# Optimization experiments

Measured on AMD Instinct MI355X. Metric: run time of the kernel, lower is better.

The kernel has to match this reference:

```python
import jax, jax.numpy as jnp
import numpy as np

T = 2048            # flattened tokens (vLLM style)
D = 4096            # hidden_size
NSSM = 128          # ssm_state_size
K = 4               # conv kernel size
G = 8               # n_groups
H = 128             # mamba_num_heads
P = 64              # mamba_head_dim
INTER = H * P       # 8192 = expand * hidden_size
CONV_DIM = INTER + 2 * G * NSSM   # 10240 (x, B, C share the conv)
PROJ = INTER + CONV_DIM + H       # 18560 (z, xBC, dt)
Q = 128             # SSD chunk size
EPS = 1e-5


def setup_inputs() -> dict:
    key = jax.random.key(0)
    ks = jax.random.split(key, 9)
    s = 0.02
    return {
        "hidden_states": jax.random.normal(ks[0], (T, D), jnp.float32),
        "residual": jax.random.normal(ks[1], (T, D), jnp.float32),
        "norm_w": jnp.ones((D,), jnp.float32),
        "in_proj_w": jax.random.normal(ks[2], (PROJ, D), jnp.float32) * s,
        "conv_w": jax.random.normal(ks[3], (CONV_DIM, K), jnp.float32) * 0.2,
        "conv_b": jax.random.normal(ks[4], (CONV_DIM,), jnp.float32) * 0.1,
        "A_log": jnp.log(jax.random.uniform(ks[5], (H,), jnp.float32, 1.0, 16.0)),
        "D_res": jax.random.normal(ks[6], (H,), jnp.float32) * 0.5 + 1.0,
        "dt_bias": jax.random.normal(ks[7], (H,), jnp.float32) * 0.5,
        "gn_w": jnp.ones((INTER,), jnp.float32),
        "out_proj_w": jax.random.normal(ks[8], (D, INTER), jnp.float32) * s,
    }


def _forward(hidden_states, residual, norm_w, in_proj_w, conv_w, conv_b,
             A_log, D_res, dt_bias, gn_w, out_proj_w):
    # ---- fused add + RMSNorm (vLLM RMSNorm(hidden, residual)) ----
    resid = hidden_states + residual
    hs = resid * jax.lax.rsqrt(jnp.mean(resid * resid, -1, keepdims=True) + EPS) * norm_w

    # ---- MambaMixer2 ----
    proj = hs @ in_proj_w.T                              # [T, PROJ]
    z, xBC, dt = jnp.split(proj, [INTER, INTER + CONV_DIM], axis=-1)

    # causal depthwise conv1d over time + SiLU
    xp = jnp.pad(xBC, ((K - 1, 0), (0, 0)))
    conv = conv_b + sum(conv_w[:, k] * xp[k:k + T] for k in range(K))
    xBC = jax.nn.silu(conv)

    x, B, C = jnp.split(xBC, [INTER, INTER + G * NSSM], axis=-1)
    x = x.reshape(T, H, P)
    Bh = jnp.repeat(B.reshape(T, G, NSSM), H // G, axis=1)   # [T,H,N]
    Ch = jnp.repeat(C.reshape(T, G, NSSM), H // G, axis=1)   # [T,H,N]

    dt = jax.nn.softplus(dt + dt_bias)                   # [T,H]
    A = -jnp.exp(A_log)                                  # [H] (negative)

    # ---- SSD chunked selective scan ----
    NC = T // Q
    a = (dt * A).reshape(NC, Q, H)                       # per-step log decay (<=0)
    cum = jnp.cumsum(a, axis=1)                          # inclusive cumsum, [NC,Q,H]
    Xd = (dt[:, :, None] * x).reshape(NC, Q, H, P)
    Bc = Bh.reshape(NC, Q, H, NSSM)
    Cc = Ch.reshape(NC, Q, H, NSSM)

    # intra-chunk: Y[i] = sum_{j<=i} (C_i.B_j) exp(cum_i-cum_j) Xd_j
    CB = jnp.einsum('cqhn,ckhn->chqk', Cc, Bc)
    cumT = cum.transpose(0, 2, 1)                        # [NC,H,Q]
    mask = jnp.tril(jnp.ones((Q, Q), bool))
    Lm = jnp.where(mask, jnp.exp(cumT[:, :, :, None] - cumT[:, :, None, :]), 0.0)
    Y = jnp.einsum('chqk,ckhp->cqhp', CB * Lm, Xd)

    # chunk-local end states, then scan states across chunks
    cum_end = cum[:, -1]                                 # [NC,H]
    decay_out = jnp.exp(cum_end[:, None] - cum)          # [NC,Q,H]
    S_loc = jnp.einsum('cqhn,cqh,cqhp->chnp', Bc, decay_out, Xd)
    chunk_decay = jnp.exp(cum_end)                       # [NC,H]

    def step(s, inp):
        dec, sl = inp
        return dec[:, None, None] * s + sl, s            # emit state BEFORE chunk

    _, S_prev = jax.lax.scan(step, jnp.zeros((H, NSSM, P), x.dtype),
                             (chunk_decay, S_loc))       # [NC,H,N,P]

    # inter-chunk contribution + skip connection D*x
    Y = Y + jnp.einsum('cqhn,cqh,chnp->cqhp', Cc, jnp.exp(cum), S_prev)
    y = Y.reshape(T, H, P) + D_res[None, :, None] * x

    # gated RMSNorm then out projection
    y = y.reshape(T, INTER) * jax.nn.silu(z)
    y = y * jax.lax.rsqrt(jnp.mean(y * y, -1, keepdims=True) + EPS) * gn_w
    return y @ out_proj_w.T, resid


def reference(hidden_states, residual, norm_w, in_proj_w, conv_w, conv_b,
              A_log, D_res, dt_bias, gn_w, out_proj_w):
    return _forward(hidden_states, residual, norm_w, in_proj_w, conv_w, conv_b,
                    A_log, D_res, dt_bias, gn_w, out_proj_w)
```

## Files before the change

kernel.cpp:

```cpp
#include <hip/hip_runtime.h>
#include <stdint.h>

typedef unsigned short u16;
typedef unsigned int   u32;
typedef float  f32x4  __attribute__((ext_vector_type(4)));
typedef __bf16 bf16x8 __attribute__((ext_vector_type(8)));
typedef u16    u16x4  __attribute__((ext_vector_type(4)));
typedef u16    u16x8  __attribute__((ext_vector_type(8)));

#define T_N     2048
#define D_N     4096
#define H_N     128
#define P_N     64
#define G_N     8
#define NS_N    128
#define INTER_N 8192
#define CONVD_N 10240
#define PROJ_N  18560
#define NGEMM_N 18432
#define NC_N    16

__device__ __forceinline__ float bf2f(u16 u){ u32 x = ((u32)u) << 16; return __builtin_bit_cast(float, x); }
__device__ __forceinline__ u16 f2bf(float f){
  u32 u = __builtin_bit_cast(u32, f);
  u += 0x7FFFu + ((u >> 16) & 1u);
  return (u16)(u >> 16);
}

__device__ __forceinline__ void gld_lds16(const void* g, void* lds){
  __builtin_amdgcn_global_load_lds(
      (const __attribute__((address_space(1))) void*)(uintptr_t)g,
      (__attribute__((address_space(3))) void*)(u32)(uintptr_t)lds,
      16, 0, 0);
}

__global__ __launch_bounds__(256)
void k_addnorm(const float* __restrict__ hin, const float* __restrict__ rin,
               const float* __restrict__ nw, float* __restrict__ resid,
               u16* __restrict__ hs16, float* __restrict__ rstd){
  __shared__ float red[4];
  const int row = blockIdx.x, tid = threadIdx.x;
  const size_t rb = (size_t)row * D_N;
  f32x4 s[4];
  float ss = 0.f;
  #pragma unroll
  for (int i = 0; i < 4; ++i){
    int c4 = tid + i*256;
    f32x4 a = *(const f32x4*)&hin[rb + (size_t)c4*4];
    f32x4 b = *(const f32x4*)&rin[rb + (size_t)c4*4];
    s[i] = a + b;
    *(f32x4*)&resid[rb + (size_t)c4*4] = s[i];
    ss += s[i][0]*s[i][0] + s[i][1]*s[i][1] + s[i][2]*s[i][2] + s[i][3]*s[i][3];
  }
  #pragma unroll
  for (int o = 32; o > 0; o >>= 1) ss += __shfl_down(ss, o, 64);
  if ((tid & 63) == 0) red[tid >> 6] = ss;
  __syncthreads();
  float tot = (red[0] + red[1]) + (red[2] + red[3]);
  float rs = rsqrtf(tot / (float)D_N + 1e-5f);
  if (tid == 0) rstd[row] = rs;
  #pragma unroll
  for (int i = 0; i < 4; ++i){
    int c4 = tid + i*256;
    f32x4 w = *(const f32x4*)&nw[(size_t)c4*4];
    u16x4 o = { f2bf(s[i][0]*rs*w[0]), f2bf(s[i][1]*rs*w[1]),
                f2bf(s[i][2]*rs*w[2]), f2bf(s[i][3]*rs*w[3]) };
    *(u16x4*)&hs16[rb + (size_t)c4*4] = o;
  }
}

__global__ void k_cvt(const float* __restrict__ in, u16* __restrict__ out, size_t n4){
  size_t i = (size_t)blockIdx.x * blockDim.x + threadIdx.x;
  size_t stride = (size_t)gridDim.x * blockDim.x;
  for (; i < n4; i += stride){
    f32x4 v = *(const f32x4*)&in[i*4];
    u16x4 o = { f2bf(v[0]), f2bf(v[1]), f2bf(v[2]), f2bf(v[3]) };
    *(u16x4*)&out[i*4] = o;
  }
}

__global__ void k_wdt(const float* __restrict__ W, const float* __restrict__ nw,
                      float* __restrict__ Wn){
  int idx = blockIdx.x*256 + threadIdx.x;
  int d = idx >> 7, h = idx & 127;
  Wn[(size_t)d*128 + h] = W[(size_t)(INTER_N + CONVD_N + h)*D_N + d] * nw[d];
}

__global__ __launch_bounds__(256)
void k_dtgemm(const float* __restrict__ resid, const float* __restrict__ Wn,
              float* __restrict__ dtpart){
  __shared__ float lhs[16*128];
  const int tid = threadIdx.x;
  const int tb = blockIdx.x >> 3, ks = blockIdx.x & 7;
  const int t0 = tb * 16;
  const int k0 = ks * (D_N / 8);
  const int hcol = tid & 127, rh = tid >> 7;
  float acc[8] = {0,0,0,0,0,0,0,0};
  for (int kt = k0; kt < k0 + D_N/8; kt += 128){
    __syncthreads();
    #pragma unroll
    for (int it = 0; it < 2; ++it){
      int idx = it*256 + tid;
      int rr = idx >> 5, c4 = idx & 31;
      *(f32x4*)&lhs[rr*128 + c4*4] = *(const f32x4*)&resid[(size_t)(t0+rr)*D_N + kt + c4*4];
    }
    __syncthreads();
    #pragma unroll 4
    for (int kk4 = 0; kk4 < 32; ++kk4){
      f32x4 w4;
      #pragma unroll
      for (int j = 0; j < 4; ++j) w4[j] = Wn[(size_t)(kt + kk4*4 + j)*128 + hcol];
      #pragma unroll
      for (int j = 0; j < 8; ++j){
        f32x4 lv = *(const f32x4*)&lhs[(rh*8 + j)*128 + kk4*4];
        acc[j] += lv[0]*w4[0] + lv[1]*w4[1] + lv[2]*w4[2] + lv[3]*w4[3];
      }
    }
  }
  #pragma unroll
  for (int j = 0; j < 8; ++j){
    int t = t0 + rh*8 + j;
    dtpart[((size_t)ks*T_N + t)*128 + hcol] = acc[j];
  }
}

__global__ void k_dtprep(const float* __restrict__ dtpart, const float* __restrict__ rstd,
                         const float* __restrict__ dt_bias, const float* __restrict__ A_log,
                         float* __restrict__ dtv, float* __restrict__ cum,
                         float* __restrict__ cumend, float* __restrict__ dec){
  int c = blockIdx.x, h = threadIdx.x;
  float A = -expf(A_log[h]);
  float bias = dt_bias[h];
  float cm = 0.f;
  for (int q = 0; q < 128; ++q){
    int t = c*128 + q;
    float s = 0.f;
    #pragma unroll
    for (int kspl = 0; kspl < 8; ++kspl)
      s += dtpart[((size_t)kspl*T_N + t)*128 + h];
    float x = s * rstd[t] + bias;
    float dv = (x > 20.f) ? x : log1pf(expf(x));
    dtv[(size_t)t*128 + h] = dv;
    cm += dv * A;
    cum[(size_t)t*128 + h] = cm;
  }
  cumend[c*128 + h] = cm;
  dec[c*128 + h] = expf(cm);
}

#define STA(BUF,HH,KT) gld_lds16(pA + (size_t)((HH)*32)*K + (size_t)(KT)*64, shb + (BUF)*BSZ + (HH)*4096 + tid*16)
#define STB(BUF,HH,KT) gld_lds16(pB + (size_t)((HH)*32)*K + (size_t)(KT)*64, shb + (BUF)*BSZ + 16384 + (HH)*4096 + tid*16)
#define VMWN do { asm volatile("s_waitcnt vmcnt(%0)" :: "n"(NF) : "memory"); __builtin_amdgcn_sched_barrier(0); } while(0)
#define RDA4(BUF, MOFF)                                                                 \
    bf16x8 a0 = *(const bf16x8*)(shb + (BUF)*BSZ + rdA + (MOFF)*2048 + sA0);            \
    bf16x8 a1 = *(const bf16x8*)(shb + (BUF)*BSZ + rdA + (MOFF)*2048 + sA1);            \
    bf16x8 a2 = *(const bf16x8*)(shb + (BUF)*BSZ + rdA + ((MOFF)+1)*2048 + sA0);        \
    bf16x8 a3 = *(const bf16x8*)(shb + (BUF)*BSZ + rdA + ((MOFF)+1)*2048 + sA1);
#define RDBALL(BUF, BB)                                                                 \
    _Pragma("unroll") for (int nn = 0; nn < NF; ++nn){                                  \
      BB[nn][0] = *(const bf16x8*)(shb + (BUF)*BSZ + rdB + nn*2048 + sA0);              \
      BB[nn][1] = *(const bf16x8*)(shb + (BUF)*BSZ + rdB + nn*2048 + sA1);              \
    }
#define MM24(MOFF, BB)                                                                  \
    _Pragma("unroll") for (int nn = 0; nn < NF; ++nn)                                   \
      acc[(MOFF)+0][nn] = __builtin_amdgcn_mfma_f32_16x16x32_bf16(a0, BB[nn][0], acc[(MOFF)+0][nn],0,0,0); \
    _Pragma("unroll") for (int nn = 0; nn < NF; ++nn)                                   \
      acc[(MOFF)+1][nn] = __builtin_amdgcn_mfma_f32_16x16x32_bf16(a2, BB[nn][0], acc[(MOFF)+1][nn],0,0,0); \
    _Pragma("unroll") for (int nn = 0; nn < NF; ++nn)                                   \
      acc[(MOFF)+0][nn] = __builtin_amdgcn_mfma_f32_16x16x32_bf16(a1, BB[nn][1], acc[(MOFF)+0][nn],0,0,0); \
    _Pragma("unroll") for (int nn = 0; nn < NF; ++nn)                                   \
      acc[(MOFF)+1][nn] = __builtin_amdgcn_mfma_f32_16x16x32_bf16(a3, BB[nn][1], acc[(MOFF)+1][nn],0,0,0);
#define ENDPH                                                                           \
    __builtin_amdgcn_s_setprio(0);                                                      \
    __builtin_amdgcn_s_barrier();                                                       \
    __builtin_amdgcn_sched_barrier(0);

template<int NF, typename OT>
__global__ __launch_bounds__(256, 2)
void k_gemmw(const u16* __restrict__ A, const u16* __restrict__ Bm,
             OT* __restrict__ C, int ldc, int K, int nkt){
  constexpr int BSZ = 16384 + NF*4096;
  __shared__ char shb[2*BSZ];
  const int tid = threadIdx.x, ln = tid & 63, wid = tid >> 6;
  const int wm = wid >> 1, wn = wid & 1;
  const int lr = ln & 15, lg = ln >> 4;

  const int gx = gridDim.x;
  const int mt = gridDim.y;
  const int lin = blockIdx.y * gx + blockIdx.x;
  const int xcd = lin & 7, sub = lin >> 3;
  const int ncx = gx >> 3;
  const int n_local = sub / mt;
  const int m_idx   = sub % mt;
  const int m0 = m_idx << 7;
  const int n0 = (xcd * ncx + n_local) * (NF*32);

  const int srow = tid >> 3;
  const int slog = ((tid & 7) ^ (srow & 7)) * 8;
  const u16* pA = A + (size_t)(m0 + srow)*K + slog;
  const u16* pB = Bm + (size_t)(n0 + srow)*K + slog;

  const int sA0 = (lg ^ (ln & 7)) << 4;
  const int sA1 = ((4 + lg) ^ (ln & 7)) << 4;
  const u32 rdA = wm*8192 + lr*128;
  const u32 rdB = 16384 + wn*(NF*2048) + lr*128;

  f32x4 acc[4][NF] = {};

  STA(0,0,0); STA(0,1,0); STA(0,2,0); STA(0,3,0);
  #pragma unroll
  for (int hh = 0; hh < NF; ++hh) STB(0, hh, 0);
  #pragma unroll
  for (int hh = 0; hh < NF; ++hh) STB(1, hh, 1);
  VMWN;
  __builtin_amdgcn_s_barrier();
  __builtin_amdgcn_sched_barrier(0);

  const int nit = nkt >> 1;
  #pragma unroll 1
  for (int it = 0; it < nit; ++it){
    const int t1 = 2*it + 1;
    int t2 = 2*it + 2; if (t2 >= nkt) t2 = 0;
    int t3 = 2*it + 3; if (t3 >= nkt) t3 = 1;
    bf16x8 bb0[NF][2], bb1[NF][2];
    {
      RDA4(0, 0) RDBALL(0, bb0)
      STA(1,0,t1); STA(1,1,t1); STA(1,2,t1); STA(1,3,t1);
      __builtin_amdgcn_s_setprio(1);
      MM24(0, bb0)
      ENDPH
    }
    {
      RDA4(0, 2)
      #pragma unroll
      for (int hh = 0; hh < NF; ++hh) STB(0, hh, t2);
      VMWN;
      __builtin_amdgcn_s_setprio(1);
      MM24(2, bb0)
      ENDPH
    }
    {
      RDA4(1, 0) RDBALL(1, bb1)
      STA(0,0,t2); STA(0,1,t2); STA(0,2,t2); STA(0,3,t2);
      __builtin_amdgcn_s_setprio(1);
      MM24(0, bb1)
      ENDPH
    }
    {
      RDA4(1, 2)
      #pragma unroll
      for (int hh = 0; hh < NF; ++hh) STB(1, hh, t3);
      VMWN;
      __builtin_amdgcn_s_setprio(1);
      MM24(2, bb1)
      ENDPH
    }
  }
  asm volatile("s_waitcnt vmcnt(0)" ::: "memory");

  const int crow = m0 + wm*64 + lg*4;
  const int ccol = n0 + wn*(NF*16) + lr;
  #pragma unroll
  for (int m = 0; m < 4; ++m)
    #pragma unroll
    for (int nn = 0; nn < NF; ++nn)
      #pragma unroll
      for (int r = 0; r < 4; ++r){
        float v = acc[m][nn][r];
        if constexpr (__is_same(OT, float))
          C[(size_t)(crow + m*16 + r)*ldc + ccol + nn*16] = v;
        else
          C[(size_t)(crow + m*16 + r)*ldc + ccol + nn*16] = f2bf(v);
      }
}

__global__ __launch_bounds__(256)
void k_conv(const u16* __restrict__ proj16, const float* __restrict__ cw,
            const float* __restrict__ cb, u16* __restrict__ x16,
            u16* __restrict__ B16, u16* __restrict__ C16){
  const int ch = blockIdx.x*256 + threadIdx.x;
  const int tbase = blockIdx.y*64;
  f32x4 w = *(const f32x4*)&cw[(size_t)ch*4];
  const float bias = cb[ch];
  const u16* pcol = proj16 + INTER_N + ch;
  float p0 = 0.f, p1 = 0.f, p2 = 0.f;
  if (tbase >= 3){
    p0 = bf2f(pcol[(size_t)(tbase-3)*PROJ_N]);
    p1 = bf2f(pcol[(size_t)(tbase-2)*PROJ_N]);
    p2 = bf2f(pcol[(size_t)(tbase-1)*PROJ_N]);
  }
  u16* xdst = (ch < INTER_N) ? x16 + ch
            : (ch < INTER_N + 1024) ? B16 + (ch - INTER_N)
            : C16 + (ch - INTER_N - 1024);
  const int dstride = (ch < INTER_N) ? INTER_N : 1024;
  #pragma unroll 4
  for (int i = 0; i < 64; ++i){
    int t = tbase + i;
    float cur = bf2f(pcol[(size_t)t*PROJ_N]);
    float acc = bias + w[0]*p0 + w[1]*p1 + w[2]*p2 + w[3]*cur;
    float v = acc / (1.f + __expf(-acc));
    xdst[(size_t)t*dstride] = f2bf(v);
    p0 = p1; p1 = p2; p2 = cur;
  }
}

__global__ __launch_bounds__(512)
void k_ssda(const u16* __restrict__ B16, const u16* __restrict__ x16,
            const float* __restrict__ dtv, const float* __restrict__ cum,
            const float* __restrict__ cumend, u16* __restrict__ SlocT){
  __shared__ u16 lBdT[128*136];
  __shared__ u16 lXdT[64*136];
  __shared__ float lDec[128], lDt[128];
  const int tid = threadIdx.x, wid = tid >> 6, ln = tid & 63;
  const int c = blockIdx.x >> 7, h = blockIdx.x & 127, g = h >> 4;
  if (tid < 128){
    int t = c*128 + tid;
    lDec[tid] = __expf(cumend[c*128 + h] - cum[(size_t)t*128 + h]);
    lDt[tid]  = dtv[(size_t)t*128 + h];
  }
  __syncthreads();
  for (int it = 0; it < 32; ++it){
    int idx = it*512 + tid;
    int q = idx >> 7, n = idx & 127;
    float bv = bf2f(B16[(size_t)(c*128 + q)*1024 + g*128 + n]) * lDec[q];
    lBdT[n*136 + q] = f2bf(bv);
  }
  for (int it = 0; it < 16; ++it){
    int idx = it*512 + tid;
    int q = idx >> 6, p = idx & 63;
    float xv = bf2f(x16[(size_t)(c*128 + q)*INTER_N + h*64 + p]) * lDt[q];
    lXdT[p*136 + q] = f2bf(xv);
  }
  __syncthreads();
  const int wr = wid >> 1, wc = wid & 1;
  const int kofs = (ln >> 4) << 3;
  f32x4 acc[2][2] = {};
  #pragma unroll
  for (int ks = 0; ks < 4; ++ks){
    bf16x8 a[2], b[2];
    #pragma unroll
    for (int m = 0; m < 2; ++m) a[m] = *(const bf16x8*)&lBdT[(wr*32 + m*16 + (ln & 15))*136 + ks*32 + kofs];
    #pragma unroll
    for (int n = 0; n < 2; ++n) b[n] = *(const bf16x8*)&lXdT[(wc*32 + n*16 + (ln & 15))*136 + ks*32 + kofs];
    #pragma unroll
    for (int m = 0; m < 2; ++m)
      #pragma unroll
      for (int n = 0; n < 2; ++n)
        acc[m][n] = __builtin_amdgcn_mfma_f32_16x16x32_bf16(a[m], b[n], acc[m][n], 0, 0, 0);
  }
  const size_t base = (size_t)(c*128 + h) * 8192;
  #pragma unroll
  for (int m = 0; m < 2; ++m)
    #pragma unroll
    for (int n = 0; n < 2; ++n){
      int p  = wc*32 + n*16 + (ln & 15);
      int nn = wr*32 + m*16 + ((ln >> 4) << 2);
      u16x4 o = { f2bf(acc[m][n][0]), f2bf(acc[m][n][1]), f2bf(acc[m][n][2]), f2bf(acc[m][n][3]) };
      *(u16x4*)&SlocT[base + (size_t)p*128 + nn] = o;
    }
}

__global__ __launch_bounds__(256)
void k_scan(const u16* __restrict__ SlocT, const float* __restrict__ dec,
            u16* __restrict__ SprevT){
  int idx = blockIdx.x*256 + threadIdx.x;
  int h = idx >> 10, p = (idx >> 4) & 63, n8 = (idx & 15)*8;
  float s[8] = {};
  for (int c = 0; c < NC_N; ++c){
    size_t off = (size_t)(c*128 + h)*8192 + (size_t)p*128 + n8;
    u16x8 o;
    #pragma unroll
    for (int j = 0; j < 8; ++j) o[j] = f2bf(s[j]);
    *(u16x8*)&SprevT[off] = o;
    u16x8 sl = *(const u16x8*)&SlocT[off];
    float d = dec[c*128 + h];
    #pragma unroll
    for (int j = 0; j < 8; ++j) s[j] = d*s[j] + bf2f(sl[j]);
  }
}

__global__ __launch_bounds__(512)
void k_ssdb(const u16* __restrict__ C16, const u16* __restrict__ B16g,
            const u16* __restrict__ x16, const float* __restrict__ dtv,
            const float* __restrict__ cum, const u16* __restrict__ SprevT,
            const u16* __restrict__ proj16, const float* __restrict__ Dres,
            u16* __restrict__ yg16){
  __shared__ u16 lC[128*136];
  __shared__ u16 lBP[128*136];
  __shared__ u16 lXdT[64*136];
  __shared__ float lCum[128], lDt[128];
  const int tid = threadIdx.x, wid = tid >> 6, ln = tid & 63;
  const int c = blockIdx.x >> 7, h = blockIdx.x & 127, g = h >> 4;
  if (tid < 128){
    int t = c*128 + tid;
    lCum[tid] = cum[(size_t)t*128 + h];
    lDt[tid]  = dtv[(size_t)t*128 + h];
  }
  __syncthreads();
  #pragma unroll
  for (int it = 0; it < 4; ++it){
    int idx = it*512 + tid;
    int q = idx >> 4, n8 = (idx & 15) << 3;
    size_t gi = (size_t)(c*128 + q)*1024 + g*128 + n8;
    *(u16x8*)&lC[q*136 + n8]  = *(const u16x8*)&C16[gi];
    *(u16x8*)&lBP[q*136 + n8] = *(const u16x8*)&B16g[gi];
  }
  for (int it = 0; it < 16; ++it){
    int idx = it*512 + tid;
    int q = idx >> 6, p = idx & 63;
    lXdT[p*136 + q] = f2bf(bf2f(x16[(size_t)(c*128 + q)*INTER_N + h*64 + p]) * lDt[q]);
  }
  __syncthreads();
  const int kofs = (ln >> 4) << 3;
  {
    const int wr = wid >> 2, wc = wid & 3;
    f32x4 cb[4][2] = {};
    #pragma unroll
    for (int ks = 0; ks < 4; ++ks){
      bf16x8 a[4], b[2];
      #pragma unroll
      for (int m = 0; m < 4; ++m) a[m] = *(const bf16x8*)&lC[(wr*64 + m*16 + (ln & 15))*136 + ks*32 + kofs];
      #pragma unroll
      for (int n = 0; n < 2; ++n) b[n] = *(const bf16x8*)&lBP[(wc*32 + n*16 + (ln & 15))*136 + ks*32 + kofs];
      #pragma unroll
      for (int m = 0; m < 4; ++m)
        #pragma unroll
        for (int n = 0; n < 2; ++n)
          cb[m][n] = __builtin_amdgcn_mfma_f32_16x16x32_bf16(a[m], b[n], cb[m][n], 0, 0, 0);
    }
    __syncthreads();
    #pragma unroll
    for (int m = 0; m < 4; ++m)
      #pragma unroll
      for (int n = 0; n < 2; ++n){
        int kcol = (wid & 3)*32 + n*16 + (ln & 15);
        float ck = lCum[kcol];
        #pragma unroll
        for (int r = 0; r < 4; ++r){
          int q = (wid >> 2)*64 + m*16 + ((ln >> 4) << 2) + r;
          float v = (kcol <= q) ? cb[m][n][r] * __expf(lCum[q] - ck) : 0.f;
          lBP[q*136 + kcol] = f2bf(v);
        }
      }
  }
  __syncthreads();
  const int yr = wid >> 1, yc = wid & 1;
  f32x4 y1[2][2] = {}, y2[2][2] = {};
  const size_t spbase = (size_t)(c*128 + h) * 8192;
  #pragma unroll
  for (int ks = 0; ks < 4; ++ks){
    bf16x8 ap[2], acf[2], bx[2], bs[2];
    #pragma unroll
    for (int m = 0; m < 2; ++m){
      int qr = yr*32 + m*16 + (ln & 15);
      ap[m]  = *(const bf16x8*)&lBP[qr*136 + ks*32 + kofs];
      acf[m] = *(const bf16x8*)&lC [qr*136 + ks*32 + kofs];
    }
    #pragma unroll
    for (int n = 0; n < 2; ++n){
      int p = yc*32 + n*16 + (ln & 15);
      bx[n] = *(const bf16x8*)&lXdT[p*136 + ks*32 + kofs];
      bs[n] = *(const bf16x8*)&SprevT[spbase + (size_t)p*128 + ks*32 + kofs];
    }
    #pragma unroll
    for (int m = 0; m < 2; ++m)
      #pragma unroll
      for (int n = 0; n < 2; ++n){
        y1[m][n] = __builtin_amdgcn_mfma_f32_16x16x32_bf16(ap[m],  bx[n], y1[m][n], 0, 0, 0);
        y2[m][n] = __builtin_amdgcn_mfma_f32_16x16x32_bf16(acf[m], bs[n], y2[m][n], 0, 0, 0);
      }
  }
  const float dh = Dres[h];
  #pragma unroll
  for (int m = 0; m < 2; ++m)
    #pragma unroll
    for (int r = 0; r < 4; ++r){
      int q = yr*32 + m*16 + ((ln >> 4) << 2) + r;
      float eq = __expf(lCum[q]);
      size_t t = (size_t)(c*128 + q);
      #pragma unroll
      for (int n = 0; n < 2; ++n){
        int p = yc*32 + n*16 + (ln & 15);
        int chn = h*64 + p;
        float xv = bf2f(x16[t*INTER_N + chn]);
        float zv = bf2f(proj16[t*PROJ_N + chn]);
        float yv = y1[m][n][r] + eq*y2[m][n][r] + dh*xv;
        float sg = zv / (1.f + __expf(-zv));
        yg16[t*INTER_N + chn] = f2bf(yv * sg);
      }
    }
}

__global__ __launch_bounds__(256)
void k_gnorm(const u16* __restrict__ yg, const float* __restrict__ gnw,
             u16* __restrict__ yn16){
  __shared__ float red[4];
  const int row = blockIdx.x, tid = threadIdx.x;
  const u16* rp = yg + (size_t)row * INTER_N;
  u16x8 v[4];
  float ss = 0.f;
  #pragma unroll
  for (int i = 0; i < 4; ++i){
    v[i] = *(const u16x8*)&rp[(size_t)(tid + i*256)*8];
    #pragma unroll
    for (int j = 0; j < 8; ++j){ float f = bf2f(v[i][j]); ss += f*f; }
  }
  #pragma unroll
  for (int o = 32; o > 0; o >>= 1) ss += __shfl_down(ss, o, 64);
  if ((tid & 63) == 0) red[tid >> 6] = ss;
  __syncthreads();
  float tot = (red[0] + red[1]) + (red[2] + red[3]);
  float sc = rsqrtf(tot / (float)INTER_N + 1e-5f);
  #pragma unroll
  for (int i = 0; i < 4; ++i){
    int c8 = (tid + i*256)*8;
    u16x8 o;
    #pragma unroll
    for (int j = 0; j < 8; ++j)
      o[j] = f2bf(bf2f(v[i][j]) * sc * gnw[c8 + j]);
    *(u16x8*)&yn16[(size_t)row*INTER_N + c8] = o;
  }
}

extern "C" void kernel_launch(void* const* d_in, const int* in_sizes, int n_in,
                              void* d_out, int out_size, void* d_ws, size_t ws_size,
                              hipStream_t stream){
  (void)in_sizes; (void)n_in; (void)out_size;
  const float* hs_in     = (const float*)d_in[0];
  const float* res_in    = (const float*)d_in[1];
  const float* norm_w    = (const float*)d_in[2];
  const float* in_proj_w = (const float*)d_in[3];
  const float* conv_w    = (const float*)d_in[4];
  const float* conv_b    = (const float*)d_in[5];
  const float* A_log     = (const float*)d_in[6];
  const float* D_res     = (const float*)d_in[7];
  const float* dt_bias   = (const float*)d_in[8];
  const float* gn_w      = (const float*)d_in[9];
  const float* out_proj_w= (const float*)d_in[10];

  float* out0      = (float*)d_out;
  float* resid_out = out0 + (size_t)T_N * D_N;

  char* ws = (char*)d_ws;
  const size_t o_hs16   = 0;
  const size_t o_Win16  = 16777216;
  const size_t o_Wout16 = 168820736;
  const size_t o_proj   = 235929600;
  const size_t o_Wn     = 387973120;
  const size_t o_dtv    = 391118848;
  const size_t o_cum    = 392167424;
  const size_t o_cumend = 393216000;
  const size_t o_dec    = 393224192;
  const size_t o_rstd   = 393232384;
  const size_t o_x16    = 393240576;
  const size_t o_B16    = 426795008;
  const size_t o_C16    = 430989312;
  const size_t o_SlocT  = 435183616;
  const size_t o_SprevT = 468738048;
  const size_t o_yn16   = 502292480;
  const size_t WS_NEED  = 535846912;
  if (ws_size < WS_NEED) return;

  u16*   hs16   = (u16*)  (ws + o_hs16);
  u16*   Win16  = (u16*)  (ws + o_Win16);
  u16*   Wout16 = (u16*)  (ws + o_Wout16);
  u16*   proj16 = (u16*)  (ws + o_proj);
  float* Wn     = (float*)(ws + o_Wn);
  float* dtpart = (float*)(ws + o_proj);
  float* dtv    = (float*)(ws + o_dtv);
  float* cum    = (float*)(ws + o_cum);
  float* cumend = (float*)(ws + o_cumend);
  float* dec    = (float*)(ws + o_dec);
  float* rstd   = (float*)(ws + o_rstd);
  u16*   x16    = (u16*)  (ws + o_x16);
  u16*   B16    = (u16*)  (ws + o_B16);
  u16*   C16    = (u16*)  (ws + o_C16);
  u16*   SlocT  = (u16*)  (ws + o_SlocT);
  u16*   SprevT = (u16*)  (ws + o_SprevT);
  u16*   yn16   = (u16*)  (ws + o_yn16);
  u16*   yg16   = (u16*)  (ws + o_Win16);

  k_addnorm<<<T_N, 256, 0, stream>>>(hs_in, res_in, norm_w, resid_out, hs16, rstd);
  k_cvt<<<4096, 256, 0, stream>>>(in_proj_w,  Win16,  (size_t)NGEMM_N * D_N / 4);
  k_cvt<<<2048, 256, 0, stream>>>(out_proj_w, Wout16, (size_t)D_N * INTER_N / 4);
  k_wdt<<<2048, 256, 0, stream>>>(in_proj_w, norm_w, Wn);
  k_dtgemm<<<1024, 256, 0, stream>>>(resid_out, Wn, dtpart);
  k_dtprep<<<NC_N, 128, 0, stream>>>(dtpart, rstd, dt_bias, A_log, dtv, cum, cumend, dec);
  k_gemmw<6, u16><<<dim3(NGEMM_N/192, T_N/128), 256, 0, stream>>>(hs16, Win16, proj16, PROJ_N, D_N, D_N/64);
  k_conv<<<dim3(CONVD_N/256, T_N/64), 256, 0, stream>>>(proj16, conv_w, conv_b, x16, B16, C16);
  k_ssda<<<NC_N * H_N, 512, 0, stream>>>(B16, x16, dtv, cum, cumend, SlocT);
  k_scan<<<512, 256, 0, stream>>>(SlocT, dec, SprevT);
  k_ssdb<<<NC_N * H_N, 512, 0, stream>>>(C16, B16, x16, dtv, cum, SprevT, proj16, D_res, yg16);
  k_gnorm<<<T_N, 256, 0, stream>>>(yg16, gn_w, yn16);
  k_gemmw<4, float><<<dim3(D_N/128, T_N/128), 256, 0, stream>>>(yn16, Wout16, out0, D_N, INTER_N, INTER_N/64);
}
```

Measured before the change: 921.8 us.

## Parallelize dt reduction, tile weight transpose via LDS, vectorize conv over channels

```diff
diff --git a/kernel.cpp b/kernel.cpp
--- a/kernel.cpp
+++ b/kernel.cpp
@@ -79,11 +79,27 @@
   }
 }
 
-__global__ void k_wdt(const float* __restrict__ W, const float* __restrict__ nw,
-                      float* __restrict__ Wn){
-  int idx = blockIdx.x*256 + threadIdx.x;
-  int d = idx >> 7, h = idx & 127;
-  Wn[(size_t)d*128 + h] = W[(size_t)(INTER_N + CONVD_N + h)*D_N + d] * nw[d];
+__global__ __launch_bounds__(256)
+void k_wdt(const float* __restrict__ W, const float* __restrict__ nw,
+           float* __restrict__ Wn){
+  __shared__ float lt[32][133];
+  const int tid = threadIdx.x;
+  const int d0 = blockIdx.x * 32;
+  #pragma unroll
+  for (int i = 0; i < 16; ++i){
+    int h = i*8 + (tid >> 5);
+    int d = tid & 31;
+    lt[d][h] = W[(size_t)(INTER_N + CONVD_N + h)*D_N + d0 + d];
+  }
+  __syncthreads();
+  #pragma unroll
+  for (int i = 0; i < 4; ++i){
+    int d = i*8 + (tid >> 5);
+    int h4 = (tid & 31) * 4;
+    float nwv = nw[d0 + d];
+    f32x4 v = { lt[d][h4]*nwv, lt[d][h4+1]*nwv, lt[d][h4+2]*nwv, lt[d][h4+3]*nwv };
+    *(f32x4*)&Wn[(size_t)(d0 + d)*128 + h4] = v;
+  }
 }
 
 __global__ __launch_bounds__(256)
@@ -124,25 +140,29 @@
   }
 }
 
-__global__ void k_dtprep(const float* __restrict__ dtpart, const float* __restrict__ rstd,
-                         const float* __restrict__ dt_bias, const float* __restrict__ A_log,
-                         float* __restrict__ dtv, float* __restrict__ cum,
+__global__ __launch_bounds__(256)
+void k_dtsum(const float* __restrict__ dtpart, const float* __restrict__ rstd,
+             const float* __restrict__ dt_bias, const float* __restrict__ A_log,
+             float* __restrict__ dtv, float* __restrict__ dta){
+  int idx = blockIdx.x*256 + threadIdx.x;
+  int t = idx >> 7, h = idx & 127;
+  float s = 0.f;
+  #pragma unroll
+  for (int k = 0; k < 8; ++k) s += dtpart[((size_t)k*T_N + t)*128 + h];
+  float x = s * rstd[t] + dt_bias[h];
+  float dv = (x > 20.f) ? x : log1pf(expf(x));
+  dtv[idx] = dv;
+  dta[idx] = dv * (-expf(A_log[h]));
+}
+
+__global__ void k_dtprep(const float* __restrict__ dta, float* __restrict__ cum,
                          float* __restrict__ cumend, float* __restrict__ dec){
   int c = blockIdx.x, h = threadIdx.x;
-  float A = -expf(A_log[h]);
-  float bias = dt_bias[h];
   float cm = 0.f;
   for (int q = 0; q < 128; ++q){
-    int t = c*128 + q;
-    float s = 0.f;
-    #pragma unroll
-    for (int kspl = 0; kspl < 8; ++kspl)
-      s += dtpart[((size_t)kspl*T_N + t)*128 + h];
-    float x = s * rstd[t] + bias;
-    float dv = (x > 20.f) ? x : log1pf(expf(x));
-    dtv[(size_t)t*128 + h] = dv;
-    cm += dv * A;
-    cum[(size_t)t*128 + h] = cm;
+    size_t i = (size_t)(c*128 + q)*128 + h;
+    cm += dta[i];
+    cum[i] = cm;
   }
   cumend[c*128 + h] = cm;
   dec[c*128 + h] = expf(cm);
@@ -223,38 +243,30 @@
     int t2 = 2*it + 2; if (t2 >= nkt) t2 = 0;
     int t3 = 2*it + 3; if (t3 >= nkt) t3 = 1;
     bf16x8 bb0[NF][2], bb1[NF][2];
-    {
-      RDA4(0, 0) RDBALL(0, bb0)
+    { RDA4(0, 0) RDBALL(0, bb0)
       STA(1,0,t1); STA(1,1,t1); STA(1,2,t1); STA(1,3,t1);
       __builtin_amdgcn_s_setprio(1);
       MM24(0, bb0)
-      ENDPH
-    }
-    {
-      RDA4(0, 2)
+      ENDPH }
+    { RDA4(0, 2)
       #pragma unroll
       for (int hh = 0; hh < NF; ++hh) STB(0, hh, t2);
       VMWN;
       __builtin_amdgcn_s_setprio(1);
       MM24(2, bb0)
-      ENDPH
-    }
-    {
-      RDA4(1, 0) RDBALL(1, bb1)
+      ENDPH }
+    { RDA4(1, 0) RDBALL(1, bb1)
       STA(0,0,t2); STA(0,1,t2); STA(0,2,t2); STA(0,3,t2);
       __builtin_amdgcn_s_setprio(1);
       MM24(0, bb1)
-      ENDPH
-    }
-    {
-      RDA4(1, 2)
+      ENDPH }
+    { RDA4(1, 2)
       #pragma unroll
       for (int hh = 0; hh < NF; ++hh) STB(1, hh, t3);
       VMWN;
       __builtin_amdgcn_s_setprio(1);
       MM24(2, bb1)
-      ENDPH
-    }
+      ENDPH }
   }
   asm volatile("s_waitcnt vmcnt(0)" ::: "memory");
 
@@ -278,29 +290,43 @@
 void k_conv(const u16* __restrict__ proj16, const float* __restrict__ cw,
             const float* __restrict__ cb, u16* __restrict__ x16,
             u16* __restrict__ B16, u16* __restrict__ C16){
-  const int ch = blockIdx.x*256 + threadIdx.x;
-  const int tbase = blockIdx.y*64;
-  f32x4 w = *(const f32x4*)&cw[(size_t)ch*4];
-  const float bias = cb[ch];
-  const u16* pcol = proj16 + INTER_N + ch;
-  float p0 = 0.f, p1 = 0.f, p2 = 0.f;
+  const int ch0 = blockIdx.x*2048 + threadIdx.x*8;
+  const int tbase = blockIdx.y*16;
+  f32x4 w[8]; float bias[8];
+  #pragma unroll
+  for (int j = 0; j < 8; ++j){
+    w[j] = *(const f32x4*)&cw[(size_t)(ch0+j)*4];
+    bias[j] = cb[ch0+j];
+  }
+  const u16* pcol = proj16 + INTER_N + ch0;
+  float p0[8], p1[8], p2[8];
   if (tbase >= 3){
-    p0 = bf2f(pcol[(size_t)(tbase-3)*PROJ_N]);
-    p1 = bf2f(pcol[(size_t)(tbase-2)*PROJ_N]);
-    p2 = bf2f(pcol[(size_t)(tbase-1)*PROJ_N]);
-  }
-  u16* xdst = (ch < INTER_N) ? x16 + ch
-            : (ch < INTER_N + 1024) ? B16 + (ch - INTER_N)
-            : C16 + (ch - INTER_N - 1024);
-  const int dstride = (ch < INTER_N) ? INTER_N : 1024;
-  #pragma unroll 4
-  for (int i = 0; i < 64; ++i){
+    u16x8 v0 = *(const u16x8*)&pcol[(size_t)(tbase-3)*PROJ_N];
+    u16x8 v1 = *(const u16x8*)&pcol[(size_t)(tbase-2)*PROJ_N];
+    u16x8 v2 = *(const u16x8*)&pcol[(size_t)(tbase-1)*PROJ_N];
+    #pragma unroll
+    for (int j = 0; j < 8; ++j){ p0[j]=bf2f(v0[j]); p1[j]=bf2f(v1[j]); p2[j]=bf2f(v2[j]); }
+  } else {
+    #pragma unroll
+    for (int j = 0; j < 8; ++j){ p0[j]=0.f; p1[j]=0.f; p2[j]=0.f; }
+  }
+  u16* xdst = (ch0 < INTER_N) ? x16 + ch0
+            : (ch0 < INTER_N + 1024) ? B16 + (ch0 - INTER_N)
+            : C16 + (ch0 - INTER_N - 1024);
+  const int dstride = (ch0 < INTER_N) ? INTER_N : 1024;
+  #pragma unroll 2
+  for (int i = 0; i < 16; ++i){
     int t = tbase + i;
-    float cur = bf2f(pcol[(size_t)t*PROJ_N]);
-    float acc = bias + w[0]*p0 + w[1]*p1 + w[2]*p2 + w[3]*cur;
-    float v = acc / (1.f + __expf(-acc));
-    xdst[(size_t)t*dstride] = f2bf(v);
-    p0 = p1; p1 = p2; p2 = cur;
+    u16x8 cv = *(const u16x8*)&pcol[(size_t)t*PROJ_N];
+    u16x8 o;
+    #pragma unroll
+    for (int j = 0; j < 8; ++j){
+      float cur = bf2f(cv[j]);
+      float a = bias[j] + w[j][0]*p0[j] + w[j][1]*p1[j] + w[j][2]*p2[j] + w[j][3]*cur;
+      o[j] = f2bf(a / (1.f + __expf(-a)));
+      p0[j] = p1[j]; p1[j] = p2[j]; p2[j] = cur;
+    }
+    *(u16x8*)&xdst[(size_t)t*dstride] = o;
   }
 }
 
@@ -567,6 +593,7 @@
   u16*   proj16 = (u16*)  (ws + o_proj);
   float* Wn     = (float*)(ws + o_Wn);
   float* dtpart = (float*)(ws + o_proj);
+  float* dta    = (float*)(ws + o_proj + (16u<<20));
   float* dtv    = (float*)(ws + o_dtv);
   float* cum    = (float*)(ws + o_cum);
   float* cumend = (float*)(ws + o_cumend);
@@ -583,11 +610,12 @@
   k_addnorm<<<T_N, 256, 0, stream>>>(hs_in, res_in, norm_w, resid_out, hs16, rstd);
   k_cvt<<<4096, 256, 0, stream>>>(in_proj_w,  Win16,  (size_t)NGEMM_N * D_N / 4);
   k_cvt<<<2048, 256, 0, stream>>>(out_proj_w, Wout16, (size_t)D_N * INTER_N / 4);
-  k_wdt<<<2048, 256, 0, stream>>>(in_proj_w, norm_w, Wn);
+  k_wdt<<<128, 256, 0, stream>>>(in_proj_w, norm_w, Wn);
   k_dtgemm<<<1024, 256, 0, stream>>>(resid_out, Wn, dtpart);
-  k_dtprep<<<NC_N, 128, 0, stream>>>(dtpart, rstd, dt_bias, A_log, dtv, cum, cumend, dec);
+  k_dtsum<<<1024, 256, 0, stream>>>(dtpart, rstd, dt_bias, A_log, dtv, dta);
+  k_dtprep<<<NC_N, 128, 0, stream>>>(dta, cum, cumend, dec);
   k_gemmw<6, u16><<<dim3(NGEMM_N/192, T_N/128), 256, 0, stream>>>(hs16, Win16, proj16, PROJ_N, D_N, D_N/64);
-  k_conv<<<dim3(CONVD_N/256, T_N/64), 256, 0, stream>>>(proj16, conv_w, conv_b, x16, B16, C16);
+  k_conv<<<dim3(CONVD_N/2048, T_N/16), 256, 0, stream>>>(proj16, conv_w, conv_b, x16, B16, C16);
   k_ssda<<<NC_N * H_N, 512, 0, stream>>>(B16, x16, dtv, cum, cumend, SlocT);
   k_scan<<<512, 256, 0, stream>>>(SlocT, dec, SprevT);
   k_ssdb<<<NC_N * H_N, 512, 0, stream>>>(C16, B16, x16, dtv, cum, SprevT, proj16, D_res, yg16);
```

Result: faster. 802.5 us (-12.9%).
